# Kernel optimization log

Hardware: AMD Instinct MI355X
Metric: run time of the kernel (lower is better)

## Reference

```python
import jax, jax.numpy as jnp
import numpy as np

B, S, D, E, R = 8, 4096, 768, 8, 8

def setup_inputs() -> dict:
    key = jax.random.key(0)
    ks = jax.random.split(key, 9)
    sc = 0.02
    return {
        "x":  jax.random.normal(ks[0], (B, S, D), dtype=jnp.float32),
        "Wd": jax.random.normal(ks[1], (E, D, R), dtype=jnp.float32) * sc,
        "bd": jax.random.normal(ks[2], (E, R), dtype=jnp.float32) * sc,
        "Wm": jax.random.normal(ks[3], (E, R, R), dtype=jnp.float32) * sc,
        "bm": jax.random.normal(ks[4], (E, R), dtype=jnp.float32) * sc,
        "Wu": jax.random.normal(ks[5], (E, R, D), dtype=jnp.float32) * sc,
        "bu": jax.random.normal(ks[6], (E, D), dtype=jnp.float32) * sc,
        "Wg": jax.random.normal(ks[7], (D, E), dtype=jnp.float32) * sc,
        "bg": jax.random.normal(ks[8], (E,), dtype=jnp.float32) * sc,
    }

def reference(x, Wd, bd, Wm, bm, Wu, bu, Wg, bg):
    # Gating: softmax over experts. [B,S,E]
    gate = jax.nn.softmax(jnp.einsum('bsd,de->bse', x, Wg) + bg, axis=-1)
    # All experts batched as 3D GEMMs (dropout = identity, eval mode).
    h = jnp.einsum('bsd,edr->bser', x, Wd) + bd            # [B,S,E,R] down
    h = jnp.einsum('bser,erq->bseq', h, Wm) + bm           # [B,S,E,R] mid
    up = jnp.einsum('bser,erd->bsed', h, Wu) + bu          # [B,S,E,D] up
    # Weighted sum over experts.
    return jnp.einsum('bse,bsed->bsd', gate, up)
```

## Files before the change

### kernel.cpp

```cpp
#include <hip/hip_runtime.h>
#include <stdint.h>


typedef short bf16x8 __attribute__((ext_vector_type(8)));
typedef float f32x4 __attribute__((ext_vector_type(4)));

static __device__ __forceinline__ unsigned short f2bf(float f) {
  union { float f; uint32_t u; } v; v.f = f;
  return (unsigned short)((v.u + 0x7fffu + ((v.u >> 16) & 1u)) >> 16);
}

__global__ void prep_weights(const float* __restrict__ Wd, const float* __restrict__ Wg,
                             const float* __restrict__ Wu, const float* __restrict__ bu,
                             unsigned short* __restrict__ w1f, unsigned short* __restrict__ w2f) {
  int tid = blockIdx.x * 256 + threadIdx.x;
  const int N1 = 24 * 5 * 64 * 8;
  if (tid < N1) {
    int i    = tid & 7;
    int lane = (tid >> 3) & 63;
    int fk   = tid >> 9;
    int f = fk % 5, K0 = fk / 5;
    int k = K0 * 32 + (lane >> 4) * 8 + i;
    int j = f * 16 + (lane & 15);
    float val = 0.f;
    if (j < 64)      val = Wd[(size_t)(j >> 3) * 6144 + (size_t)k * 8 + (j & 7)];
    else if (j < 72) val = Wg[(size_t)k * 8 + (j - 64)];
    w1f[tid] = f2bf(val);
  } else {
    int t2 = tid - N1;
    if (t2 >= 48 * 3 * 64 * 8) return;
    int i    = t2 & 7;
    int lane = (t2 >> 3) & 63;
    int tk   = t2 >> 9;
    int K0 = tk % 3, T = tk / 3;
    int k = K0 * 32 + (lane >> 4) * 8 + i;
    int n = T * 16 + (lane & 15);
    float val = 0.f;
    if (k < 64)      val = Wu[(size_t)(k >> 3) * 6144 + (size_t)(k & 7) * 768 + n];
    else if (k < 72) val = bu[(size_t)(k - 64) * 768 + n];
    w2f[t2] = f2bf(val);
  }
}

__global__ __launch_bounds__(256) void k1_g2(
    const float* __restrict__ x,
    const float* __restrict__ bd, const float* __restrict__ Wm,
    const float* __restrict__ bm, const float* __restrict__ bg,
    const unsigned short* __restrict__ w1f, unsigned int* __restrict__ g2) {
  __shared__ float Hs[4][16][81];

  const int tidx = threadIdx.x;
  const int lane = tidx & 63;
  const int wave = tidx >> 6;
  const int arow = lane & 15;
  const int kgrp = lane >> 4;
  const int tok0 = blockIdx.x * 16;

  {
    const float* xrow = x + (size_t)(tok0 + arow) * 768 + wave * 192 + kgrp * 8;
    f32x4 acc0 = {0,0,0,0}, acc1 = {0,0,0,0}, acc2 = {0,0,0,0}, acc3 = {0,0,0,0}, acc4 = {0,0,0,0};
    const bf16x8* w1v = (const bf16x8*)w1f + (size_t)(wave * 6) * 320 + lane;

    float4 xa[4][2];
    #pragma unroll
    for (int i = 0; i < 4; i++) {
      xa[i][0] = *(const float4*)(xrow + i * 32);
      xa[i][1] = *(const float4*)(xrow + i * 32 + 4);
    }
    #pragma unroll
    for (int i = 0; i < 6; i++) {
      float4 a0 = xa[i & 3][0];
      float4 a1 = xa[i & 3][1];
      if (i + 4 < 6) {
        xa[i & 3][0] = *(const float4*)(xrow + (i + 4) * 32);
        xa[i & 3][1] = *(const float4*)(xrow + (i + 4) * 32 + 4);
      }
      bf16x8 af;
      af[0] = (short)f2bf(a0.x); af[1] = (short)f2bf(a0.y);
      af[2] = (short)f2bf(a0.z); af[3] = (short)f2bf(a0.w);
      af[4] = (short)f2bf(a1.x); af[5] = (short)f2bf(a1.y);
      af[6] = (short)f2bf(a1.z); af[7] = (short)f2bf(a1.w);
      const bf16x8* bb = w1v + i * 320;
      acc0 = __builtin_amdgcn_mfma_f32_16x16x32_bf16(af, bb[0],   acc0, 0, 0, 0);
      acc1 = __builtin_amdgcn_mfma_f32_16x16x32_bf16(af, bb[64],  acc1, 0, 0, 0);
      acc2 = __builtin_amdgcn_mfma_f32_16x16x32_bf16(af, bb[128], acc2, 0, 0, 0);
      acc3 = __builtin_amdgcn_mfma_f32_16x16x32_bf16(af, bb[192], acc3, 0, 0, 0);
      acc4 = __builtin_amdgcn_mfma_f32_16x16x32_bf16(af, bb[256], acc4, 0, 0, 0);
    }
    int hr = kgrp * 4;
    #pragma unroll
    for (int r = 0; r < 4; r++) {
      Hs[wave][hr + r][arow]      = acc0[r];
      Hs[wave][hr + r][16 + arow] = acc1[r];
      Hs[wave][hr + r][32 + arow] = acc2[r];
      Hs[wave][hr + r][48 + arow] = acc3[r];
      Hs[wave][hr + r][64 + arow] = acc4[r];
    }
  }
  __syncthreads();

  if (tidx < 64) {
    int t = tidx >> 2;
    int c = tidx & 3;
    unsigned int* g2u = g2 + (size_t)(tok0 + t) * 48;
    float lg[8];
    float m = -1e30f;
    #pragma unroll
    for (int e = 0; e < 8; e++) {
      lg[e] = Hs[0][t][64 + e] + Hs[1][t][64 + e] + Hs[2][t][64 + e] + Hs[3][t][64 + e] + bg[e];
      m = fmaxf(m, lg[e]);
    }
    float den = 0.f;
    #pragma unroll
    for (int e = 0; e < 8; e++) { lg[e] = __expf(lg[e] - m); den += lg[e]; }
    float inv = 1.f / den;
    #pragma unroll
    for (int ee = 0; ee < 2; ee++) {
      int e = c * 2 + ee;
      float gate = lg[e] * inv;
      float h[8];
      #pragma unroll
      for (int r = 0; r < 8; r++)
        h[r] = Hs[0][t][e * 8 + r] + Hs[1][t][e * 8 + r] + Hs[2][t][e * 8 + r] +
               Hs[3][t][e * 8 + r] + bd[e * 8 + r];
      #pragma unroll
      for (int q = 0; q < 8; q += 2) {
        float h2a = bm[e * 8 + q], h2b = bm[e * 8 + q + 1];
        #pragma unroll
        for (int r = 0; r < 8; r++) {
          h2a += h[r] * Wm[e * 64 + r * 8 + q];
          h2b += h[r] * Wm[e * 64 + r * 8 + q + 1];
        }
        g2u[e * 4 + (q >> 1)] =
            (unsigned)f2bf(gate * h2a) | ((unsigned)f2bf(gate * h2b) << 16);
      }
    }
    g2u[32 + c] = (unsigned)f2bf(lg[c * 2] * inv) | ((unsigned)f2bf(lg[c * 2 + 1] * inv) << 16);
    g2u[36 + c * 3 + 0] = 0;
    g2u[36 + c * 3 + 1] = 0;
    g2u[36 + c * 3 + 2] = 0;
  }
}

__global__ __launch_bounds__(256) void k2_out(
    const unsigned short* __restrict__ g2bf, const unsigned short* __restrict__ w2f,
    float* __restrict__ out) {
  const int tidx = threadIdx.x;
  const int lane = tidx & 63;
  const int wave = tidx >> 6;
  const int arow = lane & 15;
  const int kgrp = lane >> 4;
  const int tok0 = blockIdx.x * 16;

  const unsigned short* grow = g2bf + (size_t)(tok0 + arow) * 96 + kgrp * 8;
  bf16x8 a2_0 = *(const bf16x8*)(grow);
  bf16x8 a2_1 = *(const bf16x8*)(grow + 32);
  bf16x8 a2_2 = *(const bf16x8*)(grow + 64);

  const bf16x8* w2v = (const bf16x8*)w2f + (size_t)(wave * 12) * 192 + lane;
  float* orow = out + (size_t)(tok0 + arow) * 768 + wave * 192 + kgrp * 4;

  bf16x8 pb[4][3];
  #pragma unroll
  for (int d = 0; d < 4; d++) {
    pb[d][0] = w2v[d * 192];
    pb[d][1] = w2v[d * 192 + 64];
    pb[d][2] = w2v[d * 192 + 128];
  }
  #pragma unroll
  for (int j = 0; j < 12; j++) {
    bf16x8 b0 = pb[j & 3][0], b1 = pb[j & 3][1], b2 = pb[j & 3][2];
    if (j + 4 < 12) {
      pb[j & 3][0] = w2v[(j + 4) * 192];
      pb[j & 3][1] = w2v[(j + 4) * 192 + 64];
      pb[j & 3][2] = w2v[(j + 4) * 192 + 128];
    }
    f32x4 c2 = {0,0,0,0};
    c2 = __builtin_amdgcn_mfma_f32_16x16x32_bf16(b0, a2_0, c2, 0, 0, 0);
    c2 = __builtin_amdgcn_mfma_f32_16x16x32_bf16(b1, a2_1, c2, 0, 0, 0);
    c2 = __builtin_amdgcn_mfma_f32_16x16x32_bf16(b2, a2_2, c2, 0, 0, 0);
    *(f32x4*)(orow + j * 16) = c2;
  }
}

extern "C" void kernel_launch(void* const* d_in, const int* in_sizes, int n_in,
                              void* d_out, int out_size, void* d_ws, size_t ws_size,
                              hipStream_t stream) {
  const float* x  = (const float*)d_in[0];
  const float* Wd = (const float*)d_in[1];
  const float* bd = (const float*)d_in[2];
  const float* Wm = (const float*)d_in[3];
  const float* bm = (const float*)d_in[4];
  const float* Wu = (const float*)d_in[5];
  const float* bu = (const float*)d_in[6];
  const float* Wg = (const float*)d_in[7];
  const float* bg = (const float*)d_in[8];
  unsigned short* w1f = (unsigned short*)d_ws;
  unsigned short* w2f = w1f + 61440;
  unsigned int*   g2  = (unsigned int*)((char*)d_ws + 270336);

  prep_weights<<<528, 256, 0, stream>>>(Wd, Wg, Wu, bu, w1f, w2f);
  k1_g2<<<2048, 256, 0, stream>>>(x, bd, Wm, bm, bg, w1f, g2);
  k2_out<<<2048, 256, 0, stream>>>((const unsigned short*)g2, w2f, (float*)d_out);
}
```

Before: 64.82 us.

## Stage x via direct global-to-LDS loads, prefetch weights, vectorize g2 and nontemporal output stores

Measured after the change: 71.00 us. 9.5% more time.

```diff
diff --git a/kernel.cpp b/kernel.cpp
--- a/kernel.cpp
+++ b/kernel.cpp
@@ -4,6 +4,13 @@
 
 typedef short bf16x8 __attribute__((ext_vector_type(8)));
 typedef float f32x4 __attribute__((ext_vector_type(4)));
+
+typedef __attribute__((address_space(3))) unsigned int lds_uint;
+typedef __attribute__((address_space(1))) unsigned int g_uint;
+
+static __device__ __forceinline__ void gload_lds16(const void* g, void* l) {
+  __builtin_amdgcn_global_load_lds((const g_uint*)g, (lds_uint*)l, 16, 0, 0);
+}
 
 static __device__ __forceinline__ unsigned short f2bf(float f) {
   union { float f; uint32_t u; } v; v.f = f;
@@ -47,6 +54,7 @@
     const float* __restrict__ bd, const float* __restrict__ Wm,
     const float* __restrict__ bm, const float* __restrict__ bg,
     const unsigned short* __restrict__ w1f, unsigned int* __restrict__ g2) {
+  __shared__ uint4 xs[4 * 12 * 64];
   __shared__ float Hs[4][16][81];
 
   const int tidx = threadIdx.x;
@@ -57,35 +65,48 @@
   const int tok0 = blockIdx.x * 16;
 
   {
-    const float* xrow = x + (size_t)(tok0 + arow) * 768 + wave * 192 + kgrp * 8;
+    const float* xsrc = x + (size_t)(tok0 + arow) * 768 + wave * 192 + kgrp * 4;
+    uint4* dst = &xs[wave * 768];
+    #pragma unroll
+    for (int j = 0; j < 12; j++)
+      gload_lds16(xsrc + j * 16, dst + j * 64);
+  }
+  asm volatile("s_waitcnt vmcnt(0)" ::: "memory");
+  __builtin_amdgcn_sched_barrier(0);
+
+  {
+    const f32x4* xs4 = (const f32x4*)xs;
+    const int wbase = wave * 768;
     f32x4 acc0 = {0,0,0,0}, acc1 = {0,0,0,0}, acc2 = {0,0,0,0}, acc3 = {0,0,0,0}, acc4 = {0,0,0,0};
     const bf16x8* w1v = (const bf16x8*)w1f + (size_t)(wave * 6) * 320 + lane;
 
-    float4 xa[4][2];
-    #pragma unroll
-    for (int i = 0; i < 4; i++) {
-      xa[i][0] = *(const float4*)(xrow + i * 32);
-      xa[i][1] = *(const float4*)(xrow + i * 32 + 4);
+    bf16x8 fb[2][5];
+    #pragma unroll
+    for (int d = 0; d < 2; d++) {
+      #pragma unroll
+      for (int q = 0; q < 5; q++) fb[d][q] = w1v[d * 320 + q * 64];
     }
     #pragma unroll
     for (int i = 0; i < 6; i++) {
-      float4 a0 = xa[i & 3][0];
-      float4 a1 = xa[i & 3][1];
-      if (i + 4 < 6) {
-        xa[i & 3][0] = *(const float4*)(xrow + (i + 4) * 32);
-        xa[i & 3][1] = *(const float4*)(xrow + (i + 4) * 32 + 4);
+      int u0 = wbase + (i * 2 + (kgrp >> 1)) * 64 + (kgrp & 1) * 32 + arow;
+      f32x4 a0 = xs4[u0];
+      f32x4 a1 = xs4[u0 + 16];
+      bf16x8 af;
+      af[0] = (short)f2bf(a0[0]); af[1] = (short)f2bf(a0[1]);
+      af[2] = (short)f2bf(a0[2]); af[3] = (short)f2bf(a0[3]);
+      af[4] = (short)f2bf(a1[0]); af[5] = (short)f2bf(a1[1]);
+      af[6] = (short)f2bf(a1[2]); af[7] = (short)f2bf(a1[3]);
+      bf16x8 b0 = fb[i & 1][0], b1 = fb[i & 1][1], b2 = fb[i & 1][2],
+             b3 = fb[i & 1][3], b4 = fb[i & 1][4];
+      if (i + 2 < 6) {
+        #pragma unroll
+        for (int q = 0; q < 5; q++) fb[i & 1][q] = w1v[(i + 2) * 320 + q * 64];
       }
-      bf16x8 af;
-      af[0] = (short)f2bf(a0.x); af[1] = (short)f2bf(a0.y);
-      af[2] = (short)f2bf(a0.z); af[3] = (short)f2bf(a0.w);
-      af[4] = (short)f2bf(a1.x); af[5] = (short)f2bf(a1.y);
-      af[6] = (short)f2bf(a1.z); af[7] = (short)f2bf(a1.w);
-      const bf16x8* bb = w1v + i * 320;
-      acc0 = __builtin_amdgcn_mfma_f32_16x16x32_bf16(af, bb[0],   acc0, 0, 0, 0);
-      acc1 = __builtin_amdgcn_mfma_f32_16x16x32_bf16(af, bb[64],  acc1, 0, 0, 0);
-      acc2 = __builtin_amdgcn_mfma_f32_16x16x32_bf16(af, bb[128], acc2, 0, 0, 0);
-      acc3 = __builtin_amdgcn_mfma_f32_16x16x32_bf16(af, bb[192], acc3, 0, 0, 0);
-      acc4 = __builtin_amdgcn_mfma_f32_16x16x32_bf16(af, bb[256], acc4, 0, 0, 0);
+      acc0 = __builtin_amdgcn_mfma_f32_16x16x32_bf16(af, b0, acc0, 0, 0, 0);
+      acc1 = __builtin_amdgcn_mfma_f32_16x16x32_bf16(af, b1, acc1, 0, 0, 0);
+      acc2 = __builtin_amdgcn_mfma_f32_16x16x32_bf16(af, b2, acc2, 0, 0, 0);
+      acc3 = __builtin_amdgcn_mfma_f32_16x16x32_bf16(af, b3, acc3, 0, 0, 0);
+      acc4 = __builtin_amdgcn_mfma_f32_16x16x32_bf16(af, b4, acc4, 0, 0, 0);
     }
     int hr = kgrp * 4;
     #pragma unroll
@@ -114,6 +135,7 @@
     #pragma unroll
     for (int e = 0; e < 8; e++) { lg[e] = __expf(lg[e] - m); den += lg[e]; }
     float inv = 1.f / den;
+    unsigned int hv[8];
     #pragma unroll
     for (int ee = 0; ee < 2; ee++) {
       int e = c * 2 + ee;
@@ -131,10 +153,12 @@
           h2a += h[r] * Wm[e * 64 + r * 8 + q];
           h2b += h[r] * Wm[e * 64 + r * 8 + q + 1];
         }
-        g2u[e * 4 + (q >> 1)] =
+        hv[ee * 4 + (q >> 1)] =
             (unsigned)f2bf(gate * h2a) | ((unsigned)f2bf(gate * h2b) << 16);
       }
     }
+    *(uint4*)(g2u + 8 * c)     = make_uint4(hv[0], hv[1], hv[2], hv[3]);
+    *(uint4*)(g2u + 8 * c + 4) = make_uint4(hv[4], hv[5], hv[6], hv[7]);
     g2u[32 + c] = (unsigned)f2bf(lg[c * 2] * inv) | ((unsigned)f2bf(lg[c * 2 + 1] * inv) << 16);
     g2u[36 + c * 3 + 0] = 0;
     g2u[36 + c * 3 + 1] = 0;
@@ -179,7 +203,7 @@
     c2 = __builtin_amdgcn_mfma_f32_16x16x32_bf16(b0, a2_0, c2, 0, 0, 0);
     c2 = __builtin_amdgcn_mfma_f32_16x16x32_bf16(b1, a2_1, c2, 0, 0, 0);
     c2 = __builtin_amdgcn_mfma_f32_16x16x32_bf16(b2, a2_2, c2, 0, 0, 0);
-    *(f32x4*)(orow + j * 16) = c2;
+    __builtin_nontemporal_store(c2, (f32x4*)(orow + j * 16));
   }
 }
 
```
